# Performance work log

Measured on AMD Instinct MI355X. Metric: run time of the kernel, lower is better.

## Reference

```python
import jax, jax.numpy as jnp
import numpy as np

EPS = 1e-05
NUM_HEADS = 8
NUM_GROUPS = 32  # min(32, 512 // 4)


def setup_inputs() -> dict:
    key = jax.random.key(0)
    ks = jax.random.split(key, 5)
    B, C, T, X = 4, 512, 16, 2048
    return {
        "x": jax.random.normal(ks[0], (B, C, T, X), dtype=jnp.float32),
        "gn_w": jnp.ones((C,), dtype=jnp.float32),
        "gn_b": jnp.zeros((C,), dtype=jnp.float32),
        "qkv_w": jax.random.normal(ks[1], (3 * C, C), dtype=jnp.float32) * 0.02,
        "qkv_b": jax.random.normal(ks[2], (3 * C,), dtype=jnp.float32) * 0.02,
        "proj_w": jax.random.normal(ks[3], (C, C), dtype=jnp.float32) * 1e-5,
        "proj_b": jnp.zeros((C,), dtype=jnp.float32),
        "pos_emb": jax.random.normal(ks[4], (NUM_HEADS, 2 * T), dtype=jnp.float32) * 1e-5,
    }


def _group_norm(x, w, b):
    B, C, T, X = x.shape
    g = NUM_GROUPS
    xg = x.reshape(B, g, C // g, T, X)
    mu = xg.mean(axis=(2, 3, 4), keepdims=True)
    var = ((xg - mu) ** 2).mean(axis=(2, 3, 4), keepdims=True)
    xn = ((xg - mu) * jax.lax.rsqrt(var + EPS)).reshape(B, C, T, X)
    return xn * w[None, :, None, None] + b[None, :, None, None]


def reference(x, gn_w, gn_b, qkv_w, qkv_b, proj_w, proj_b, pos_emb):
    dtype = x.dtype
    x = x.astype(jnp.float32)
    B, C, T, X = x.shape
    H = NUM_HEADS
    hc = C // H

    xn = _group_norm(x, gn_w, gn_b)
    # 1x1 conv == channel matmul: [B, 3C, T, X]
    qkv = jnp.einsum('oc,bctx->botx', qkv_w, xn) + qkv_b[None, :, None, None]
    # 'b (n heads c) t x -> n (b x) heads t c'
    qkv = qkv.reshape(B, 3, H, hc, T, X)
    qkv = qkv.transpose(1, 0, 5, 2, 4, 3).reshape(3, B * X, H, T, hc)
    q, k, v = qkv[0], qkv[1], qkv[2]

    scale = 1.0 / np.sqrt(hc)
    attn = jnp.einsum('bhqc,bhkc->bhqk', q, k * scale)  # [(B X), H, T, T]

    i = jnp.arange(T)
    pairwise = i[:, None] - i[None, :] + T - 1        # [T, T] in [0, 2T-2]
    rel = pos_emb[:, pairwise]                         # [H, T, T]

    w = jax.nn.softmax(attn + rel[None], axis=-1)
    out = jnp.einsum('bhqk,bhkc->bhcq', w, v)          # [(B X), H, hc, T]
    # '(b x) h c t -> b (h c) t x'
    out = out.reshape(B, X, H, hc, T).transpose(0, 2, 3, 4, 1).reshape(B, C, T, X)

    y = jnp.einsum('oc,bctx->botx', proj_w, out) + proj_b[None, :, None, None]
    return y.astype(dtype)
```

## Files before the change

### kernel.cpp

```cpp
#include <hip/hip_runtime.h>
#include <math.h>

#define EPSV 1e-5f

typedef _Float16 f16;
typedef _Float16 f16x8 __attribute__((ext_vector_type(8)));
typedef _Float16 f16x4 __attribute__((ext_vector_type(4)));
typedef float f32x4 __attribute__((ext_vector_type(4)));

typedef const __attribute__((address_space(1))) void* as1_cvp;
typedef __attribute__((address_space(3))) void* as3_vp;
__device__ __forceinline__ void load_lds16(const void* g, void* l) {
    __builtin_amdgcn_global_load_lds((as1_cvp)g, (as3_vp)l, 16, 0, 0);
}

static constexpr int GROUP_N = 16 * 16 * 2048;

__global__ __launch_bounds__(256) void k_gn_part(const float* __restrict__ x,
                                                 float* __restrict__ psum,
                                                 float* __restrict__ psq) {
    const int blk = blockIdx.x;
    const int tid = threadIdx.x;
    const float* p = x + (size_t)blk * 32768;
    float s = 0.f, q = 0.f;
#pragma unroll
    for (int i = 0; i < 32; ++i) {
        float4 v = *(const float4*)(p + (size_t)(i * 256 + tid) * 4);
        s += v.x + v.y + v.z + v.w;
        q += v.x * v.x + v.y * v.y + v.z * v.z + v.w * v.w;
    }
#pragma unroll
    for (int off = 32; off > 0; off >>= 1) {
        s += __shfl_down(s, off);
        q += __shfl_down(q, off);
    }
    __shared__ float ls[4], lq[4];
    const int wave = tid >> 6, lane = tid & 63;
    if (lane == 0) { ls[wave] = s; lq[wave] = q; }
    __syncthreads();
    if (tid == 0) {
        psum[blk] = ls[0] + ls[1] + ls[2] + ls[3];
        psq[blk]  = lq[0] + lq[1] + lq[2] + lq[3];
    }
}

__global__ void k_gn_final(const float* __restrict__ psum, const float* __restrict__ psq,
                           float* __restrict__ mu, float* __restrict__ rs) {
    const int t = threadIdx.x;
    float s = 0.f, q = 0.f;
#pragma unroll
    for (int i = 0; i < 16; ++i) { s += psum[t * 16 + i]; q += psq[t * 16 + i]; }
    const float m = s / (float)GROUP_N;
    float v = q / (float)GROUP_N - m * m;
    mu[t] = m;
    rs[t] = 1.0f / sqrtf(v + EPSV);
}

__global__ __launch_bounds__(256) void k_fold_sc(const float* __restrict__ gn_w,
                                                 const float* __restrict__ gn_b,
                                                 const float* __restrict__ mu,
                                                 const float* __restrict__ rs,
                                                 float* __restrict__ sc,
                                                 float* __restrict__ beta) {
    const int u = blockIdx.x * 256 + threadIdx.x;
    const int b = u >> 9, c = u & 511;
    const int g = c >> 4;
    const float r = rs[b * 32 + g], m = mu[b * 32 + g];
    const float s = r * gn_w[c];
    sc[u]   = s;
    beta[u] = gn_b[c] - m * s;
}

__global__ __launch_bounds__(256) void k_fold_bias(const float* __restrict__ qkv_w,
                                                   const float* __restrict__ qkv_b,
                                                   const float* __restrict__ beta,
                                                   float* __restrict__ qbias) {
    const int u = blockIdx.x * 256 + threadIdx.x;
    const int b = u / 1536, o = u % 1536;
    float acc = qkv_b[o];
    const float* wr = qkv_w + (size_t)o * 512;
    const float* be = beta + b * 512;
#pragma unroll 4
    for (int c = 0; c < 512; c += 4) {
        float4 w4 = *(const float4*)(wr + c);
        float4 b4 = *(const float4*)(be + c);
        acc += w4.x * b4.x + w4.y * b4.y + w4.z * b4.z + w4.w * b4.w;
    }
    if (o >= 512 && o < 1024) acc *= 0.125f;
    qbias[u] = acc;
}


__global__ __launch_bounds__(256) void k_prep_w(const float* __restrict__ qkv_w,
                                                const float* __restrict__ proj_w,
                                                f16* __restrict__ w16,
                                                f16* __restrict__ p16) {
    const int id = blockIdx.x * 256 + threadIdx.x;
    if (id < 196608) {
        const int e0 = id * 4;
        const int o  = e0 >> 9;
        const float ksc = (o >= 512 && o < 1024) ? 0.125f : 1.0f;
        float4 v = *(const float4*)(qkv_w + e0);
        f16x4 h = { (f16)(v.x * ksc), (f16)(v.y * ksc), (f16)(v.z * ksc), (f16)(v.w * ksc) };
        *(f16x4*)(w16 + e0) = h;
    } else {
        const int e0 = (id - 196608) * 4;
        float4 v = *(const float4*)(proj_w + e0);
        f16x4 h = { (f16)v.x, (f16)v.y, (f16)v.z, (f16)v.w };
        *(f16x4*)(p16 + e0) = h;
    }
}

__global__ __launch_bounds__(256) void k_xt(const float* __restrict__ x,
                                            const float* __restrict__ sc,
                                            const float* __restrict__ beta,
                                            f16* __restrict__ xT) {
    const int x0 = blockIdx.x * 64;
    const int c0 = blockIdx.y * 64;
    const int b  = blockIdx.z >> 4, t = blockIdx.z & 15;
    const int tid = threadIdx.x;
    __shared__ float tile[64][68];
#pragma unroll
    for (int it = 0; it < 4; ++it) {
        int idx = it * 256 + tid;
        int c = idx >> 4, xq = idx & 15;
        int cg = c0 + c;
        float s = sc[b * 512 + cg], be = beta[b * 512 + cg];
        float4 v = *(const float4*)(x + (((size_t)(b * 512 + cg) * 16 + t) * 2048) + x0 + xq * 4);
        tile[c][xq * 4 + 0] = v.x * s + be;
        tile[c][xq * 4 + 1] = v.y * s + be;
        tile[c][xq * 4 + 2] = v.z * s + be;
        tile[c][xq * 4 + 3] = v.w * s + be;
    }
    __syncthreads();
#pragma unroll
    for (int it = 0; it < 2; ++it) {
        int idx = it * 256 + tid;
        int xr = idx >> 3, ch = idx & 7;
        f16x8 h;
#pragma unroll
        for (int e = 0; e < 8; ++e) h[e] = (f16)tile[ch * 8 + e][xr];
        *(f16x8*)(xT + (((size_t)(b * 2048 + x0 + xr) * 16 + t) * 512) + c0 + ch * 8) = h;
    }
}

__global__ __launch_bounds__(256) void k3_mfma(const f16* __restrict__ xT,
                                               const f16* __restrict__ w16,
                                               const float* __restrict__ qkv_b,
                                               const float* __restrict__ pos_emb,
                                               float* __restrict__ out) {
    extern __shared__ __attribute__((aligned(16))) char smem[];
    const int h  = blockIdx.x;
    const int x0 = blockIdx.y * 8;
    const int b  = blockIdx.z;
    const int tid = threadIdx.x;
    const int lane = tid & 63, w = tid >> 6;
    const int wm = w >> 1, wn = w & 1;
    const int t_l = lane & 15, g = lane >> 4;

    const f16* xTb = xT + ((size_t)b * 2048 + x0) * 16 * 512;

    const int l8 = lane >> 3;
    const int gc = (lane & 7) ^ l8;

    f32x4 acc[6][4];
#pragma unroll
    for (int mi = 0; mi < 6; ++mi)
#pragma unroll
        for (int ni = 0; ni < 4; ++ni) acc[mi][ni] = (f32x4){0.f, 0.f, 0.f, 0.f};

    {
#pragma unroll
        for (int i = 0; i < 6; ++i) {
            int m0 = (w * 6 + i) * 8;
            int m = m0 + l8;
            int o = (m >> 6) * 512 + h * 64 + (m & 63);
            load_lds16(w16 + (size_t)o * 512 + gc * 8, smem + m0 * 128);
        }
#pragma unroll
        for (int i = 0; i < 4; ++i) {
            int n0 = (w * 4 + i) * 8;
            int n = n0 + l8;
            load_lds16(xTb + (size_t)n * 512 + gc * 8, smem + 24576 + n0 * 128);
        }
    }
    __syncthreads();

    int cur = 0;
    for (int ks = 0; ks < 8; ++ks) {
        if (ks < 7) {
            char* bufn = smem + (cur ^ 1) * 40960;
            const int kon = (ks + 1) * 64;
#pragma unroll
            for (int i = 0; i < 6; ++i) {
                int m0 = (w * 6 + i) * 8;
                int m = m0 + l8;
                int o = (m >> 6) * 512 + h * 64 + (m & 63);
                load_lds16(w16 + (size_t)o * 512 + kon + gc * 8, bufn + m0 * 128);
            }
#pragma unroll
            for (int i = 0; i < 4; ++i) {
                int n0 = (w * 4 + i) * 8;
                int n = n0 + l8;
                load_lds16(xTb + (size_t)n * 512 + kon + gc * 8, bufn + 24576 + n0 * 128);
            }
        }
        const char* bufc = smem + cur * 40960;
        const f16* a_s = (const f16*)bufc;
        const f16* b_s = (const f16*)(bufc + 24576);
#pragma unroll
        for (int kk = 0; kk < 2; ++kk) {
            const int kb = kk * 4 + g;
            f16x8 af[6], bf[4];
#pragma unroll
            for (int mi = 0; mi < 6; ++mi) {
                int m = wm * 96 + mi * 16 + t_l;
                af[mi] = *(const f16x8*)(a_s + m * 64 + ((kb ^ (m & 7)) * 8));
            }
#pragma unroll
            for (int ni = 0; ni < 4; ++ni) {
                int n = wn * 64 + ni * 16 + t_l;
                bf[ni] = *(const f16x8*)(b_s + n * 64 + ((kb ^ (n & 7)) * 8));
            }
#pragma unroll
            for (int mi = 0; mi < 6; ++mi)
#pragma unroll
                for (int ni = 0; ni < 4; ++ni)
                    acc[mi][ni] = __builtin_amdgcn_mfma_f32_16x16x32_f16(af[mi], bf[ni], acc[mi][ni], 0, 0, 0);
        }
        __syncthreads();
        cur ^= 1;
    }

#pragma unroll
    for (int mi = 0; mi < 6; ++mi)
#pragma unroll
        for (int ni = 0; ni < 4; ++ni) {
            int n  = wn * 64 + ni * 16 + t_l;
            int mb = wm * 96 + mi * 16 + g * 4;
            int byte_off = n * 512 + (((mb >> 6) * 8 + (((mb >> 3) & 7) ^ (n & 7))) * 16) + (mb & 7) * 2;
            f16x4 hv;
#pragma unroll
            for (int r2 = 0; r2 < 4; ++r2) {
                int row = mb + r2;
                int reg = row >> 6;
                float qb = qkv_b[reg * 512 + h * 64 + (row & 63)];
                if (reg == 1) qb *= 0.125f;
                hv[r2] = (f16)(acc[mi][ni][r2] + qb);
            }
            *(f16x4*)(smem + byte_off) = hv;
        }
    __syncthreads();

#pragma unroll
    for (int xc = 0; xc < 2; ++xc) {
        const int xx = w * 2 + xc;
        const int nb = xx * 16;
        const int nrow = nb + t_l;
        const int rbase = nrow * 512;
        const int sw = nrow & 7;

        f32x4 s_acc = {0.f, 0.f, 0.f, 0.f};
#pragma unroll
        for (int half = 0; half < 2; ++half) {
            int qiA = (g + 4 * half) & 7;
            f16x8 afr = *(const f16x8*)(smem + rbase + ((8 + (qiA ^ sw)) * 16));
            f16x8 bfr = *(const f16x8*)(smem + rbase + ((qiA ^ sw) * 16));
            s_acc = __builtin_amdgcn_mfma_f32_16x16x32_f16(afr, bfr, s_acc, 0, 0, 0);
        }
        float sv[4];
#pragma unroll
        for (int r2 = 0; r2 < 4; ++r2)
            sv[r2] = s_acc[r2] + pos_emb[h * 32 + t_l - (g * 4 + r2) + 15];
        float mx = fmaxf(fmaxf(sv[0], sv[1]), fmaxf(sv[2], sv[3]));
        mx = fmaxf(mx, __shfl_xor(mx, 16));
        mx = fmaxf(mx, __shfl_xor(mx, 32));
        float es[4], ssum = 0.f;
#pragma unroll
        for (int r2 = 0; r2 < 4; ++r2) { es[r2] = __expf(sv[r2] - mx); ssum += es[r2]; }
        ssum += __shfl_xor(ssum, 16);
        ssum += __shfl_xor(ssum, 32);
        const float inv = 1.0f / ssum;
        f16x4 pfrag;
#pragma unroll
        for (int r2 = 0; r2 < 4; ++r2) pfrag[r2] = (f16)(es[r2] * inv);

        f32x4 o_acc[4];
#pragma unroll
        for (int cb = 0; cb < 4; ++cb) {
            int mV = 128 + cb * 16 + t_l;
            int qiV = (mV >> 3) & 7;
            f16x4 vfrag;
#pragma unroll
            for (int jj = 0; jj < 4; ++jj) {
                int nV = nb + g * 4 + jj;
                vfrag[jj] = *(const f16*)(smem + nV * 512 + ((16 + (qiV ^ (nV & 7))) * 16) + (mV & 7) * 2);
            }
            f32x4 z = {0.f, 0.f, 0.f, 0.f};
            o_acc[cb] = __builtin_amdgcn_mfma_f32_16x16x16f16(vfrag, pfrag, z, 0, 0, 0);
        }
#pragma unroll
        for (int cb = 0; cb < 4; ++cb) {
            int qd = cb * 4 + g;
            int byte_off = rbase + (((qd >> 3) * 8 + ((qd & 7) ^ sw)) * 16);
            *(f32x4*)(smem + byte_off) = o_acc[cb];
        }
    }
    __syncthreads();

    const int c = tid & 63, tq = tid >> 6;
    const int qc = c >> 2;
#pragma unroll
    for (int ti = 0; ti < 4; ++ti) {
        int t = tq * 4 + ti;
        float vals[8];
#pragma unroll
        for (int xx = 0; xx < 8; ++xx) {
            int n2 = xx * 16 + t;
            vals[xx] = *(const float*)(smem + n2 * 512 + (((qc >> 3) * 8 + ((qc & 7) ^ (n2 & 7))) * 16) + (c & 3) * 4);
        }
        float4 lo = {vals[0], vals[1], vals[2], vals[3]};
        float4 hi = {vals[4], vals[5], vals[6], vals[7]};
        size_t oaddr = (((size_t)b * 512 + h * 64 + c) * 16 + t) * 2048 + x0;
        *(float4*)(out + oaddr) = lo;
        *(float4*)(out + oaddr + 4) = hi;
    }
}

__global__ __launch_bounds__(256) void k4_mfma(const f16* __restrict__ p16,
                                               const float* __restrict__ pb,
                                               float* __restrict__ io) {
    const int x0 = blockIdx.x * 64;
    const int t  = blockIdx.y;
    const int b  = blockIdx.z;
    const int tid = threadIdx.x, lane = tid & 63, w = tid >> 6;

    __shared__ __attribute__((aligned(16))) char smem4[81920];
    f16* in_sT = (f16*)smem4;
    f16* bp_s  = (f16*)(smem4 + 65536);

    const size_t base_in = (((size_t)b * 512) * 16 + t) * 2048 + x0;
#pragma unroll
    for (int it = 0; it < 32; ++it) {
        int s = it * 256 + tid;
        int c = s >> 4, xq = s & 15;
        float4 v = *(const float4*)(io + base_in + (size_t)c * 16 * 2048 + xq * 4);
        int kc = c >> 3, j = c & 7;
        float vv[4] = {v.x, v.y, v.z, v.w};
#pragma unroll
        for (int e = 0; e < 4; ++e) {
            int xx = xq * 4 + e;
            in_sT[xx * 512 + ((kc ^ (xx & 7)) * 8) + j] = (f16)vv[e];
        }
    }

    for (int no = 0; no < 4; ++no) {
        const int o_base = no * 128;
        f32x4 acc[4][2];
#pragma unroll
        for (int mi = 0; mi < 4; ++mi)
#pragma unroll
            for (int nj = 0; nj < 2; ++nj) acc[mi][nj] = (f32x4){0.f, 0.f, 0.f, 0.f};

        for (int ko = 0; ko < 8; ++ko) {
            __syncthreads();
#pragma unroll
            for (int it = 0; it < 4; ++it) {
                int s = it * 256 + tid;
                int orow = s >> 3, ch = s & 7;
                uint4 v = *(const uint4*)(p16 + (size_t)(o_base + orow) * 512 + ko * 64 + ch * 8);
                *(uint4*)(bp_s + orow * 64 + ((ch ^ (orow & 7)) * 8)) = v;
            }
            __syncthreads();
#pragma unroll
            for (int kk = 0; kk < 2; ++kk) {
                const int kb4 = kk * 4 + (lane >> 4);
                f16x8 af[4], bf[2];
#pragma unroll
                for (int mi = 0; mi < 4; ++mi) {
                    int xx = mi * 16 + (lane & 15);
                    int kc = ko * 8 + kb4;
                    af[mi] = *(const f16x8*)(in_sT + xx * 512 + ((kc ^ (xx & 7)) * 8));
                }
#pragma unroll
                for (int nj = 0; nj < 2; ++nj) {
                    int orow = w * 32 + nj * 16 + (lane & 15);
                    bf[nj] = *(const f16x8*)(bp_s + orow * 64 + ((kb4 ^ (orow & 7)) * 8));
                }
#pragma unroll
                for (int mi = 0; mi < 4; ++mi)
#pragma unroll
                    for (int nj = 0; nj < 2; ++nj)
                        acc[mi][nj] = __builtin_amdgcn_mfma_f32_16x16x32_f16(af[mi], bf[nj], acc[mi][nj], 0, 0, 0);
            }
        }
#pragma unroll
        for (int mi = 0; mi < 4; ++mi)
#pragma unroll
            for (int nj = 0; nj < 2; ++nj) {
                int o = o_base + w * 32 + nj * 16 + (lane & 15);
                int xxb = mi * 16 + (lane >> 4) * 4;
                float bias = pb[o];
                float4 ov = {acc[mi][nj][0] + bias, acc[mi][nj][1] + bias,
                             acc[mi][nj][2] + bias, acc[mi][nj][3] + bias};
                *(float4*)(io + (((size_t)b * 512 + o) * 16 + t) * 2048 + x0 + xxb) = ov;
            }
    }
}


__global__ __launch_bounds__(256) void k_qkv_attn(const float* __restrict__ x,
                                                  const float* __restrict__ qkv_w,
                                                  const float* __restrict__ sc,
                                                  const float* __restrict__ qbias,
                                                  const float* __restrict__ pos_emb,
                                                  float* __restrict__ out) {
    const int h  = blockIdx.x;
    const int x0 = blockIdx.y * 4;
    const int b  = blockIdx.z;
    const int tid = threadIdx.x;

    __shared__ float a_s[192][68];
    __shared__ float b_s[64][68];
    __shared__ float w_s[4][16][17];

    const int ty = tid >> 3;
    const int tx = tid & 7;

    float acc[6][8];
#pragma unroll
    for (int j = 0; j < 6; ++j)
#pragma unroll
        for (int k = 0; k < 8; ++k) acc[j][k] = 0.f;

    for (int ko = 0; ko < 512; ko += 64) {
        __syncthreads();
#pragma unroll
        for (int it = 0; it < 12; ++it) {
            int idx = it * 256 + tid;
            int m = idx >> 4;
            int c4 = (idx & 15) * 4;
            int g = m >> 6, i = m & 63;
            int o = g * 512 + h * 64 + i;
            float4 w4 = *(const float4*)(qkv_w + (size_t)o * 512 + ko + c4);
            float4 s4 = *(const float4*)(sc + b * 512 + ko + c4);
            float ksc = (g == 1) ? 0.125f : 1.0f;
            float4 v;
            v.x = w4.x * s4.x * ksc; v.y = w4.y * s4.y * ksc;
            v.z = w4.z * s4.z * ksc; v.w = w4.w * s4.w * ksc;
            *(float4*)&a_s[m][c4] = v;
        }
#pragma unroll
        for (int it = 0; it < 4; ++it) {
            int idx = it * 256 + tid;
            int cc = idx >> 4, t = idx & 15;
            float4 v = *(const float4*)(x + ((size_t)((b * 512 + ko + cc) * 16 + t)) * 2048 + x0);
            *(float4*)&b_s[cc][t * 4] = v;
        }
        __syncthreads();
#pragma unroll 4
        for (int cc = 0; cc < 64; ++cc) {
            float av[6];
#pragma unroll
            for (int j = 0; j < 6; ++j) av[j] = a_s[ty * 6 + j][cc];
            float4 b0 = *(const float4*)&b_s[cc][tx * 8];
            float4 b1 = *(const float4*)&b_s[cc][tx * 8 + 4];
            float bv[8] = {b0.x, b0.y, b0.z, b0.w, b1.x, b1.y, b1.z, b1.w};
#pragma unroll
            for (int j = 0; j < 6; ++j)
#pragma unroll
                for (int k = 0; k < 8; ++k)
                    acc[j][k] = fmaf(av[j], bv[k], acc[j][k]);
        }
    }
#pragma unroll
    for (int j = 0; j < 6; ++j) {
        int m = ty * 6 + j;
        int o = (m >> 6) * 512 + h * 64 + (m & 63);
        float qb = qbias[b * 1536 + o];
#pragma unroll
        for (int k = 0; k < 8; ++k) acc[j][k] += qb;
    }
    __syncthreads();
#pragma unroll
    for (int j = 0; j < 6; ++j)
#pragma unroll
        for (int k = 0; k < 8; ++k)
            a_s[ty * 6 + j][tx * 8 + k] = acc[j][k];
    __syncthreads();

    {
        const int xx = tid >> 6;
        const int t  = (tid >> 2) & 15;
        const int uq = tid & 3;
        float l[4] = {0.f, 0.f, 0.f, 0.f};
        for (int i = 0; i < 64; ++i) {
            float qv = a_s[i][t * 4 + xx];
#pragma unroll
            for (int uu = 0; uu < 4; ++uu)
                l[uu] = fmaf(qv, a_s[64 + i][(uq * 4 + uu) * 4 + xx], l[uu]);
        }
#pragma unroll
        for (int uu = 0; uu < 4; ++uu) {
            int u = uq * 4 + uu;
            w_s[xx][t][u] = l[uu] + pos_emb[h * 32 + t - u + 15];
        }
    }
    __syncthreads();
    if (tid < 64) {
        const int xx = tid >> 4, t = tid & 15;
        float mx = -3.4e38f;
#pragma unroll
        for (int u = 0; u < 16; ++u) mx = fmaxf(mx, w_s[xx][t][u]);
        float ssum = 0.f;
#pragma unroll
        for (int u = 0; u < 16; ++u) {
            float e = __expf(w_s[xx][t][u] - mx);
            w_s[xx][t][u] = e;
            ssum += e;
        }
        float inv = 1.0f / ssum;
#pragma unroll
        for (int u = 0; u < 16; ++u) w_s[xx][t][u] *= inv;
    }
    __syncthreads();
    {
        const int i  = tid & 63;
        const int t4 = tid >> 6;
        float4 varr[16];
#pragma unroll
        for (int u = 0; u < 16; ++u) varr[u] = *(const float4*)&a_s[128 + i][u * 4];
#pragma unroll
        for (int tt = 0; tt < 4; ++tt) {
            int t = t4 * 4 + tt;
            float4 o4 = {0.f, 0.f, 0.f, 0.f};
#pragma unroll
            for (int u = 0; u < 16; ++u) {
                o4.x = fmaf(w_s[0][t][u], varr[u].x, o4.x);
                o4.y = fmaf(w_s[1][t][u], varr[u].y, o4.y);
                o4.z = fmaf(w_s[2][t][u], varr[u].z, o4.z);
                o4.w = fmaf(w_s[3][t][u], varr[u].w, o4.w);
            }
            *(float4*)(out + ((size_t)((b * 512 + h * 64 + i) * 16 + t)) * 2048 + x0) = o4;
        }
    }
}

__global__ __launch_bounds__(256) void k_proj(const float* __restrict__ pw,
                                              const float* __restrict__ pb,
                                              float* __restrict__ io) {
    const int n0 = blockIdx.x * 32;
    const int b  = blockIdx.y;
    const int tid = threadIdx.x;
    __shared__ float in_s[512][36];
    __shared__ float w_s[128][65];

    {
        const float* src = io + (size_t)b * 512 * 32768 + n0;
#pragma unroll
        for (int it = 0; it < 64; ++it) {
            int idx = it * 256 + tid;
            int r = idx >> 5, j = idx & 31;
            in_s[r][j] = src[(size_t)r * 32768 + j];
        }
    }
    __syncthreads();

    const int ty = tid >> 3;
    const int tx = tid & 7;

    for (int mo = 0; mo < 512; mo += 128) {
        float acc[4][4];
#pragma unroll
        for (int j = 0; j < 4; ++j)
#pragma unroll
            for (int k = 0; k < 4; ++k) acc[j][k] = 0.f;

        for (int ko = 0; ko < 512; ko += 64) {
#pragma unroll
            for (int it = 0; it < 32; ++it) {
                int idx = it * 256 + tid;
                int m = idx >> 6, cc = idx & 63;
                w_s[m][cc] = pw[(size_t)(mo + m) * 512 + ko + cc];
            }
            __syncthreads();
#pragma unroll 4
            for (int cc = 0; cc < 64; ++cc) {
                float4 bv = *(const float4*)&in_s[ko + cc][tx * 4];
                float a0 = w_s[ty * 4 + 0][cc];
                float a1 = w_s[ty * 4 + 1][cc];
                float a2 = w_s[ty * 4 + 2][cc];
                float a3 = w_s[ty * 4 + 3][cc];
                acc[0][0] = fmaf(a0, bv.x, acc[0][0]); acc[0][1] = fmaf(a0, bv.y, acc[0][1]);
                acc[0][2] = fmaf(a0, bv.z, acc[0][2]); acc[0][3] = fmaf(a0, bv.w, acc[0][3]);
                acc[1][0] = fmaf(a1, bv.x, acc[1][0]); acc[1][1] = fmaf(a1, bv.y, acc[1][1]);
                acc[1][2] = fmaf(a1, bv.z, acc[1][2]); acc[1][3] = fmaf(a1, bv.w, acc[1][3]);
                acc[2][0] = fmaf(a2, bv.x, acc[2][0]); acc[2][1] = fmaf(a2, bv.y, acc[2][1]);
                acc[2][2] = fmaf(a2, bv.z, acc[2][2]); acc[2][3] = fmaf(a2, bv.w, acc[2][3]);
                acc[3][0] = fmaf(a3, bv.x, acc[3][0]); acc[3][1] = fmaf(a3, bv.y, acc[3][1]);
                acc[3][2] = fmaf(a3, bv.z, acc[3][2]); acc[3][3] = fmaf(a3, bv.w, acc[3][3]);
            }
            __syncthreads();
        }
#pragma unroll
        for (int j = 0; j < 4; ++j) {
            int m = mo + ty * 4 + j;
            float bias = pb[m];
            float4 o4 = {acc[j][0] + bias, acc[j][1] + bias, acc[j][2] + bias, acc[j][3] + bias};
            *(float4*)(io + (size_t)(b * 512 + m) * 32768 + n0 + tx * 4) = o4;
        }
    }
}

extern "C" void kernel_launch(void* const* d_in, const int* in_sizes, int n_in,
                              void* d_out, int out_size, void* d_ws, size_t ws_size,
                              hipStream_t stream) {
    (void)in_sizes; (void)n_in; (void)out_size;
    const float* x       = (const float*)d_in[0];
    const float* gn_w    = (const float*)d_in[1];
    const float* gn_b    = (const float*)d_in[2];
    const float* qkv_w   = (const float*)d_in[3];
    const float* qkv_b   = (const float*)d_in[4];
    const float* proj_w  = (const float*)d_in[5];
    const float* proj_b  = (const float*)d_in[6];
    const float* pos_emb = (const float*)d_in[7];
    float* out = (float*)d_out;

    float* ws    = (float*)d_ws;
    float* psum  = ws;
    float* psq   = ws + 2048;
    float* mu    = ws + 4096;
    float* rs    = ws + 4224;
    float* sc    = ws + 4352;
    float* beta  = ws + 6400;
    float* qbias = ws + 8448;

    const size_t W16_OFF = 65536;
    const size_t P16_OFF = W16_OFF + (size_t)1536 * 512 * 2;
    const size_t XT_OFF  = P16_OFF + (size_t)512 * 512 * 2;
    const size_t NEEDED  = XT_OFF + (size_t)4 * 2048 * 16 * 512 * 2;

    k_gn_part<<<dim3(2048), dim3(256), 0, stream>>>(x, psum, psq);
    k_gn_final<<<dim3(1), dim3(128), 0, stream>>>(psum, psq, mu, rs);
    k_fold_sc<<<dim3(8), dim3(256), 0, stream>>>(gn_w, gn_b, mu, rs, sc, beta);

    const int K3_LDS = 81920;
    hipError_t attr_ok = hipFuncSetAttribute((const void*)k3_mfma,
                                             hipFuncAttributeMaxDynamicSharedMemorySize,
                                             K3_LDS);

    if (ws_size >= NEEDED && attr_ok == hipSuccess) {
        f16* w16 = (f16*)((char*)d_ws + W16_OFF);
        f16* p16 = (f16*)((char*)d_ws + P16_OFF);
        f16* xT  = (f16*)((char*)d_ws + XT_OFF);
        k_prep_w<<<dim3(1024), dim3(256), 0, stream>>>(qkv_w, proj_w, w16, p16);
        k_xt<<<dim3(32, 8, 64), dim3(256), 0, stream>>>(x, sc, beta, xT);
        k3_mfma<<<dim3(8, 256, 4), dim3(256), K3_LDS, stream>>>(xT, w16, qkv_b, pos_emb, out);
        k4_mfma<<<dim3(32, 16, 4), dim3(256), 0, stream>>>(p16, proj_b, out);
    } else {
        k_fold_bias<<<dim3(24), dim3(256), 0, stream>>>(qkv_w, qkv_b, beta, qbias);
        k_qkv_attn<<<dim3(8, 512, 4), dim3(256), 0, stream>>>(x, qkv_w, sc, qbias, pos_emb, out);
        k_proj<<<dim3(1024, 4), dim3(256), 0, stream>>>(proj_w, proj_b, out);
    }
}
```

Baseline: 640.9 us.

## Write attention output as fp16 transposed buffer and add matching projection GEMM

The attention kernel can now write its per-head output directly as fp16 into a token-major, channel-contiguous workspace buffer, skipping the LDS transpose and the fp32 store to the output tensor. A new projection kernel reads that buffer with async global-to-LDS loads and double buffering, runs an MFMA GEMM against the fp16 projection weights, and writes the fp32 NCTX output with bias. The aim is to cut intermediate traffic to half width and make the projection loads contiguous. In exchange it needs an extra 128MB workspace, and the new path only runs when the workspace is large enough; otherwise the old path is used.

```diff
diff --git a/kernel.cpp b/kernel.cpp
--- a/kernel.cpp
+++ b/kernel.cpp
@@ -148,7 +148,8 @@
                                                const f16* __restrict__ w16,
                                                const float* __restrict__ qkv_b,
                                                const float* __restrict__ pos_emb,
-                                               float* __restrict__ out) {
+                                               float* __restrict__ out,
+                                               f16* __restrict__ aT) {
     extern __shared__ __attribute__((aligned(16))) char smem[];
     const int h  = blockIdx.x;
     const int x0 = blockIdx.y * 8;
@@ -299,31 +300,153 @@
             f32x4 z = {0.f, 0.f, 0.f, 0.f};
             o_acc[cb] = __builtin_amdgcn_mfma_f32_16x16x16f16(vfrag, pfrag, z, 0, 0, 0);
         }
-#pragma unroll
-        for (int cb = 0; cb < 4; ++cb) {
-            int qd = cb * 4 + g;
-            int byte_off = rbase + (((qd >> 3) * 8 + ((qd & 7) ^ sw)) * 16);
-            *(f32x4*)(smem + byte_off) = o_acc[cb];
-        }
-    }
-    __syncthreads();
-
-    const int c = tid & 63, tq = tid >> 6;
-    const int qc = c >> 2;
-#pragma unroll
-    for (int ti = 0; ti < 4; ++ti) {
-        int t = tq * 4 + ti;
-        float vals[8];
-#pragma unroll
-        for (int xx = 0; xx < 8; ++xx) {
-            int n2 = xx * 16 + t;
-            vals[xx] = *(const float*)(smem + n2 * 512 + (((qc >> 3) * 8 + ((qc & 7) ^ (n2 & 7))) * 16) + (c & 3) * 4);
-        }
-        float4 lo = {vals[0], vals[1], vals[2], vals[3]};
-        float4 hi = {vals[4], vals[5], vals[6], vals[7]};
-        size_t oaddr = (((size_t)b * 512 + h * 64 + c) * 16 + t) * 2048 + x0;
-        *(float4*)(out + oaddr) = lo;
-        *(float4*)(out + oaddr + 4) = hi;
+        if (aT) {
+            f16* dst = aT + (((size_t)(b * 2048 + x0 + xx) * 16) + t_l) * 512 + h * 64;
+#pragma unroll
+            for (int cb = 0; cb < 4; ++cb) {
+                f16x4 hv;
+#pragma unroll
+                for (int r2 = 0; r2 < 4; ++r2) hv[r2] = (f16)o_acc[cb][r2];
+                *(f16x4*)(dst + cb * 16 + g * 4) = hv;
+            }
+        } else {
+#pragma unroll
+            for (int cb = 0; cb < 4; ++cb) {
+                int qd = cb * 4 + g;
+                int byte_off = rbase + (((qd >> 3) * 8 + ((qd & 7) ^ sw)) * 16);
+                *(f32x4*)(smem + byte_off) = o_acc[cb];
+            }
+        }
+    }
+    if (!aT) {
+        __syncthreads();
+        const int c = tid & 63, tq = tid >> 6;
+        const int qc = c >> 2;
+#pragma unroll
+        for (int ti = 0; ti < 4; ++ti) {
+            int t = tq * 4 + ti;
+            float vals[8];
+#pragma unroll
+            for (int xx = 0; xx < 8; ++xx) {
+                int n2 = xx * 16 + t;
+                vals[xx] = *(const float*)(smem + n2 * 512 + (((qc >> 3) * 8 + ((qc & 7) ^ (n2 & 7))) * 16) + (c & 3) * 4);
+            }
+            float4 lo = {vals[0], vals[1], vals[2], vals[3]};
+            float4 hi = {vals[4], vals[5], vals[6], vals[7]};
+            size_t oaddr = (((size_t)b * 512 + h * 64 + c) * 16 + t) * 2048 + x0;
+            *(float4*)(out + oaddr) = lo;
+            *(float4*)(out + oaddr + 4) = hi;
+        }
+    }
+}
+
+__global__ __launch_bounds__(256) void k4x(const f16* __restrict__ attnT,
+                                           const f16* __restrict__ p16,
+                                           const float* __restrict__ pb,
+                                           float* __restrict__ out) {
+    extern __shared__ __attribute__((aligned(16))) char smem[];
+    const int oc  = blockIdx.x;
+    const int win = blockIdx.y;
+    const int b   = blockIdx.z;
+    const int tid = threadIdx.x;
+    const int lane = tid & 63, w = tid >> 6;
+    const int t_l = lane & 15, g = lane >> 4;
+    const int l8 = lane >> 3;
+    const int gc = (lane & 7) ^ l8;
+
+    const f16* Bb = attnT + ((size_t)b * 2048 + win * 16) * 16 * 512;
+    const f16* Ab = p16 + (size_t)oc * 64 * 512;
+
+    f32x4 acc[4][4];
+#pragma unroll
+    for (int mi = 0; mi < 4; ++mi)
+#pragma unroll
+        for (int ni = 0; ni < 4; ++ni) acc[mi][ni] = (f32x4){0.f, 0.f, 0.f, 0.f};
+
+    {
+#pragma unroll
+        for (int i = 0; i < 2; ++i) {
+            int m0 = w * 16 + i * 8;
+            load_lds16(Ab + (size_t)(m0 + l8) * 512 + gc * 8, smem + m0 * 128);
+        }
+#pragma unroll
+        for (int i = 0; i < 8; ++i) {
+            int n0 = w * 64 + i * 8;
+            load_lds16(Bb + (size_t)(n0 + l8) * 512 + gc * 8, smem + 8192 + n0 * 128);
+        }
+    }
+    __syncthreads();
+
+    int cur = 0;
+    for (int ks = 0; ks < 8; ++ks) {
+        if (ks < 7) {
+            char* bufn = smem + (cur ^ 1) * 40960;
+            const int kon = (ks + 1) * 64;
+#pragma unroll
+            for (int i = 0; i < 2; ++i) {
+                int m0 = w * 16 + i * 8;
+                load_lds16(Ab + (size_t)(m0 + l8) * 512 + kon + gc * 8, bufn + m0 * 128);
+            }
+#pragma unroll
+            for (int i = 0; i < 8; ++i) {
+                int n0 = w * 64 + i * 8;
+                load_lds16(Bb + (size_t)(n0 + l8) * 512 + kon + gc * 8, bufn + 8192 + n0 * 128);
+            }
+        }
+        const char* bufc = smem + cur * 40960;
+        const f16* a_s = (const f16*)bufc;
+        const f16* b_s = (const f16*)(bufc + 8192);
+#pragma unroll
+        for (int kk = 0; kk < 2; ++kk) {
+            const int kb = kk * 4 + g;
+            f16x8 af[4], bf[4];
+#pragma unroll
+            for (int mi = 0; mi < 4; ++mi) {
+                int m = mi * 16 + t_l;
+                af[mi] = *(const f16x8*)(a_s + m * 64 + ((kb ^ (m & 7)) * 8));
+            }
+#pragma unroll
+            for (int ni = 0; ni < 4; ++ni) {
+                int n = w * 64 + ni * 16 + t_l;
+                bf[ni] = *(const f16x8*)(b_s + n * 64 + ((kb ^ (n & 7)) * 8));
+            }
+#pragma unroll
+            for (int mi = 0; mi < 4; ++mi)
+#pragma unroll
+                for (int ni = 0; ni < 4; ++ni)
+                    acc[mi][ni] = __builtin_amdgcn_mfma_f32_16x16x32_f16(af[mi], bf[ni], acc[mi][ni], 0, 0, 0);
+        }
+        __syncthreads();
+        cur ^= 1;
+    }
+
+    float* y_s = (float*)smem;
+#pragma unroll
+    for (int mi = 0; mi < 4; ++mi)
+#pragma unroll
+        for (int ni = 0; ni < 4; ++ni) {
+            int nn = w * 64 + ni * 16 + t_l;
+            int xx = nn >> 4, tt = nn & 15;
+            int ob = mi * 16 + g * 4;
+#pragma unroll
+            for (int r2 = 0; r2 < 4; ++r2)
+                y_s[(ob + r2) * 273 + xx * 17 + tt] = acc[mi][ni][r2];
+        }
+    __syncthreads();
+#pragma unroll
+    for (int k = 0; k < 4; ++k) {
+        int pair = k * 256 + tid;
+        int o = pair >> 4, t = pair & 15;
+        float bias = pb[oc * 64 + o];
+        float v[16];
+#pragma unroll
+        for (int xx = 0; xx < 16; ++xx) v[xx] = y_s[o * 273 + xx * 17 + t] + bias;
+        size_t addr = (((size_t)b * 512 + oc * 64 + o) * 16 + t) * 2048 + win * 16;
+#pragma unroll
+        for (int v4 = 0; v4 < 4; ++v4) {
+            float4 ov = {v[v4 * 4 + 0], v[v4 * 4 + 1], v[v4 * 4 + 2], v[v4 * 4 + 3]};
+            *(float4*)(out + addr + v4 * 4) = ov;
+        }
     }
 }
 
@@ -638,25 +761,34 @@
     const size_t W16_OFF = 65536;
     const size_t P16_OFF = W16_OFF + (size_t)1536 * 512 * 2;
     const size_t XT_OFF  = P16_OFF + (size_t)512 * 512 * 2;
-    const size_t NEEDED  = XT_OFF + (size_t)4 * 2048 * 16 * 512 * 2;
+    const size_t AT_OFF  = XT_OFF + (size_t)4 * 2048 * 16 * 512 * 2;
+    const size_t NEEDED  = AT_OFF;
+    const size_t NEEDED2 = AT_OFF + (size_t)4 * 2048 * 16 * 512 * 2;
 
     k_gn_part<<<dim3(2048), dim3(256), 0, stream>>>(x, psum, psq);
     k_gn_final<<<dim3(1), dim3(128), 0, stream>>>(psum, psq, mu, rs);
     k_fold_sc<<<dim3(8), dim3(256), 0, stream>>>(gn_w, gn_b, mu, rs, sc, beta);
 
     const int K3_LDS = 81920;
-    hipError_t attr_ok = hipFuncSetAttribute((const void*)k3_mfma,
-                                             hipFuncAttributeMaxDynamicSharedMemorySize,
-                                             K3_LDS);
-
-    if (ws_size >= NEEDED && attr_ok == hipSuccess) {
+    hipError_t a1 = hipFuncSetAttribute((const void*)k3_mfma,
+                                        hipFuncAttributeMaxDynamicSharedMemorySize, K3_LDS);
+    hipError_t a2 = hipFuncSetAttribute((const void*)k4x,
+                                        hipFuncAttributeMaxDynamicSharedMemorySize, K3_LDS);
+
+    if (ws_size >= NEEDED && a1 == hipSuccess) {
         f16* w16 = (f16*)((char*)d_ws + W16_OFF);
         f16* p16 = (f16*)((char*)d_ws + P16_OFF);
         f16* xT  = (f16*)((char*)d_ws + XT_OFF);
         k_prep_w<<<dim3(1024), dim3(256), 0, stream>>>(qkv_w, proj_w, w16, p16);
         k_xt<<<dim3(32, 8, 64), dim3(256), 0, stream>>>(x, sc, beta, xT);
-        k3_mfma<<<dim3(8, 256, 4), dim3(256), K3_LDS, stream>>>(xT, w16, qkv_b, pos_emb, out);
-        k4_mfma<<<dim3(32, 16, 4), dim3(256), 0, stream>>>(p16, proj_b, out);
+        if (ws_size >= NEEDED2 && a2 == hipSuccess) {
+            f16* attnT = (f16*)((char*)d_ws + AT_OFF);
+            k3_mfma<<<dim3(8, 256, 4), dim3(256), K3_LDS, stream>>>(xT, w16, qkv_b, pos_emb, out, attnT);
+            k4x<<<dim3(8, 128, 4), dim3(256), K3_LDS, stream>>>(attnT, p16, proj_b, out);
+        } else {
+            k3_mfma<<<dim3(8, 256, 4), dim3(256), K3_LDS, stream>>>(xT, w16, qkv_b, pos_emb, out, nullptr);
+            k4_mfma<<<dim3(32, 16, 4), dim3(256), 0, stream>>>(p16, proj_b, out);
+        }
     } else {
         k_fold_bias<<<dim3(24), dim3(256), 0, stream>>>(qkv_w, qkv_b, beta, qbias);
         k_qkv_attn<<<dim3(8, 512, 4), dim3(256), 0, stream>>>(x, qkv_w, sc, qbias, pos_emb, out);
```

New measurement: 614.0 us. 1.04x faster.
